# Performance work log

Measured on AMD Instinct MI355X. Metric: run time of the kernel, lower is better.

Reference implementation:

```python
import jax, jax.numpy as jnp
import numpy as np

WIDTH = 128


def setup_inputs() -> dict:
    key = jax.random.key(0)
    k_logits, k_w1, k_b1, k_w2, k_b2 = jax.random.split(key, 5)
    B, T, V = 32, 256, 4096
    logits = jax.random.normal(k_logits, (B, T, V), dtype=jnp.float32)
    # Linear(1, width): weight [width, 1] -> stored transposed as [1, width]
    w1 = jax.random.normal(k_w1, (1, WIDTH), dtype=jnp.float32) / jnp.sqrt(1.0)
    b1 = jax.random.normal(k_b1, (WIDTH,), dtype=jnp.float32) * 0.1
    # Linear(width, 1): weight [1, width] -> stored transposed as [width, 1]
    w2 = jax.random.normal(k_w2, (WIDTH, 1), dtype=jnp.float32) / jnp.sqrt(WIDTH)
    b2 = jax.random.normal(k_b2, (1,), dtype=jnp.float32) * 0.1
    return {"logits": logits, "w1": w1, "b1": b1, "w2": w2, "b2": b2}


def reference(logits, w1, b1, w2, b2):
    B, T, V = logits.shape
    logits_trim = logits[:, :-1, :]                       # [B, T-1, V]
    # entropy of softmax over the class dim; logits - logsumexp == log_softmax
    logp = jax.nn.log_softmax(logits_trim, axis=-1)       # [B, T-1, V]
    p = jnp.exp(logp)
    entropy = -jnp.sum(p * logp, axis=-1, keepdims=True)  # [B, T-1, 1]
    entropy_max = jnp.log(jnp.asarray(T, dtype=logits.dtype))  # log(num_steps)
    norm = 2.0 * entropy / entropy_max - 1.0              # [B, T-1, 1]
    # tiny 1 -> width -> 1 MLP
    hidden = jax.nn.relu(norm @ w1 + b1)                  # [B, T-1, width]
    lin = (2.0 * hidden) @ w2 + b2                        # [B, T-1, 1]
    # ns = [T-1, T-2, ..., 1]
    ns = jnp.arange(T - 1, 0, -1, dtype=logits.dtype).reshape(1, T - 1, 1)
    flags_trim = jax.nn.sigmoid(lin - jnp.log(ns))        # [B, T-1, 1]
    zeros = jnp.zeros((B, 1, 1), dtype=logits.dtype)
    ones = jnp.ones((B, 1, 1), dtype=logits.dtype)
    flags = jnp.concatenate([zeros, flags_trim, ones], axis=1)  # [B, T+1, 1]
    probabilities = jax.nn.softmax(logits, axis=2)        # [B, T, V]
    residuals = jnp.cumprod(1.0 - flags[:, :-1], axis=1)  # [B, T, 1] survival
    frequencies = probabilities * flags[:, 1:] * residuals  # [B, T, V]
    return frequencies
```

## Files before the change

### kernel.cpp

```cpp
#include <hip/hip_runtime.h>
#include <math.h>

#define T_DIM 256
#define V_DIM 4096
#define WIDTH 128

__device__ __forceinline__ float wave_max_f(float v) {
#pragma unroll
  for (int o = 32; o > 0; o >>= 1) v = fmaxf(v, __shfl_xor(v, o));
  return v;
}

__device__ __forceinline__ float wave_sum_f(float v) {
#pragma unroll
  for (int o = 32; o > 0; o >>= 1) v += __shfl_xor(v, o);
  return v;
}

__device__ __forceinline__ double wave_sum_d(double v) {
#pragma unroll
  for (int o = 32; o > 0; o >>= 1) v += __shfl_xor(v, o);
  return v;
}

__global__ __launch_bounds__(256) void row_stats(
    const float* __restrict__ logits,
    const float* __restrict__ w1, const float* __restrict__ b1,
    const float* __restrict__ w2, const float* __restrict__ b2,
    float* __restrict__ row_max, double* __restrict__ row_Z,
    double* __restrict__ row_flag) {
  const int row = blockIdx.x;
  const int t = row & (T_DIM - 1);
  const int tid = threadIdx.x;
  const int lane = tid & 63;
  const int wave = tid >> 6;

  const float4* src = (const float4*)(logits + (size_t)row * V_DIM);
  float4 xv[4];
#pragma unroll
  for (int k = 0; k < 4; ++k) xv[k] = src[tid + k * 256];

  float m = -INFINITY;
#pragma unroll
  for (int k = 0; k < 4; ++k)
    m = fmaxf(m, fmaxf(fmaxf(xv[k].x, xv[k].y), fmaxf(xv[k].z, xv[k].w)));
  m = wave_max_f(m);

  __shared__ float smax[4];
  __shared__ float szs[4], sss[4];
  if (lane == 0) smax[wave] = m;
  __syncthreads();
  m = fmaxf(fmaxf(smax[0], smax[1]), fmaxf(smax[2], smax[3]));

  float z = 0.f, s = 0.f;
#pragma unroll
  for (int k = 0; k < 4; ++k) {
    float vals[4] = {xv[k].x, xv[k].y, xv[k].z, xv[k].w};
#pragma unroll
    for (int j = 0; j < 4; ++j) {
      float sv = vals[j] - m;
      float ev = expf(sv);
      z += ev;
      s = fmaf(ev, sv, s);
    }
  }
  z = wave_sum_f(z);
  s = wave_sum_f(s);
  if (lane == 0) { szs[wave] = z; sss[wave] = s; }
  __syncthreads();

  if (wave == 0 && lane == 0) {
    double zd = (double)szs[0] + szs[1] + szs[2] + szs[3];
    double sd = (double)sss[0] + sss[1] + sss[2] + sss[3];
    row_max[row] = m;
    row_Z[row] = zd;
    if (t < T_DIM - 1) {
      double H = log(zd) - sd / zd;
      double nrm = 2.0 * H / log(256.0) - 1.0;
      double acc = 0.0;
#pragma unroll 4
      for (int j = 0; j < WIDTH; ++j) {
        double h = nrm * (double)w1[j] + (double)b1[j];
        h = h > 0.0 ? h : 0.0;
        acc += h * (double)w2[j];
      }
      double lin = 2.0 * acc + (double)b2[0];
      double xx = lin - log((double)(T_DIM - 1 - t));
      row_flag[row] = 1.0 / (1.0 + exp(-xx));
    }
  }
}

__global__ __launch_bounds__(64) void cumprod_scan(
    const double* __restrict__ row_Z, const double* __restrict__ row_flag,
    float* __restrict__ row_scale) {
  const int b = blockIdx.x;
  const int lane = threadIdx.x;
  __shared__ double fl[T_DIM];

  const double* fb = row_flag + (size_t)b * T_DIM;
  const double* Zb = row_Z + (size_t)b * T_DIM;

#pragma unroll
  for (int j = lane; j < T_DIM; j += 64) fl[j] = (j == T_DIM - 1) ? 1.0 : fb[j];
  __syncthreads();

  double loc[4];
  double p = 1.0;
#pragma unroll
  for (int j = 0; j < 4; ++j) {
    int t = lane * 4 + j;
    double flag_t = (t == 0) ? 0.0 : fl[t - 1];
    p *= (1.0 - flag_t);
    loc[j] = p;
  }
  double inc = p;
#pragma unroll
  for (int o = 1; o < 64; o <<= 1) {
    double up = __shfl_up(inc, o);
    if (lane >= o) inc *= up;
  }
  double exc = __shfl_up(inc, 1);
  if (lane == 0) exc = 1.0;

#pragma unroll
  for (int j = 0; j < 4; ++j) {
    int t = lane * 4 + j;
    double resid = exc * loc[j];
    row_scale[(size_t)b * T_DIM + t] = (float)(fl[t] * resid / Zb[t]);
  }
}

__global__ __launch_bounds__(256) void out_k(const float* __restrict__ logits,
                                             const float* __restrict__ row_max,
                                             const float* __restrict__ row_scale,
                                             float* __restrict__ out) {
  const int row = blockIdx.x;
  const int tid = threadIdx.x;
  const float m = row_max[row];
  const float sc = row_scale[row];
  const float4* src = (const float4*)(logits + (size_t)row * V_DIM);
  float4* dst = (float4*)(out + (size_t)row * V_DIM);
#pragma unroll
  for (int k = 0; k < 4; ++k) {
    float4 x = src[tid + k * 256];
    float4 o;
    o.x = expf(x.x - m) * sc;
    o.y = expf(x.y - m) * sc;
    o.z = expf(x.z - m) * sc;
    o.w = expf(x.w - m) * sc;
    dst[tid + k * 256] = o;
  }
}

extern "C" void kernel_launch(void* const* d_in, const int* in_sizes, int n_in,
                              void* d_out, int out_size, void* d_ws, size_t ws_size,
                              hipStream_t stream) {
  const float* logits = (const float*)d_in[0];
  const float* w1 = (const float*)d_in[1];
  const float* b1 = (const float*)d_in[2];
  const float* w2 = (const float*)d_in[3];
  const float* b2 = (const float*)d_in[4];
  float* out = (float*)d_out;

  const size_t nrows = (size_t)in_sizes[0] / V_DIM;
  const int Bn = (int)(nrows / T_DIM);

  double* row_Z = (double*)d_ws;
  double* row_flag = row_Z + nrows;
  float* row_max = (float*)(row_flag + nrows);
  float* row_scale = row_max + nrows;

  row_stats<<<(int)nrows, 256, 0, stream>>>(logits, w1, b1, w2, b2,
                                            row_max, row_Z, row_flag);
  cumprod_scan<<<Bn, 64, 0, stream>>>(row_Z, row_flag, row_scale);
  out_k<<<(int)nrows, 256, 0, stream>>>(logits, row_max, row_scale, out);
}
```

Before: 263.5 us.

## Fuse three kernels into one cooperative persistent kernel with grid syncs

Replaces the row-stats, cumprod-scan and output kernels with a single cooperative kernel of 512 blocks, each handling 16 rows, separated by two grid-wide syncs. The MLP flag computation is moved from one thread per row to 16 threads per block running in parallel, and output stores use nontemporal hints. The aim is to remove launch gaps and the serial tail of many tiny kernels. The cost is fewer resident blocks, so less latency hiding on the 134 MB streaming passes, plus the overhead of the grid barriers.

```diff
diff --git a/kernel.cpp b/kernel.cpp
--- a/kernel.cpp
+++ b/kernel.cpp
@@ -1,155 +1,160 @@
 #include <hip/hip_runtime.h>
+#include <hip/hip_cooperative_groups.h>
 #include <math.h>
+
+namespace cg = cooperative_groups;
 
 #define T_DIM 256
 #define V_DIM 4096
 #define WIDTH 128
+#define NBLK 512
+#define ROWS_PER_BLK 16
+
+typedef float floatx4 __attribute__((ext_vector_type(4)));
 
 __device__ __forceinline__ float wave_max_f(float v) {
 #pragma unroll
   for (int o = 32; o > 0; o >>= 1) v = fmaxf(v, __shfl_xor(v, o));
   return v;
 }
-
 __device__ __forceinline__ float wave_sum_f(float v) {
 #pragma unroll
   for (int o = 32; o > 0; o >>= 1) v += __shfl_xor(v, o);
   return v;
 }
 
-__device__ __forceinline__ double wave_sum_d(double v) {
-#pragma unroll
-  for (int o = 32; o > 0; o >>= 1) v += __shfl_xor(v, o);
-  return v;
-}
-
-__global__ __launch_bounds__(256) void row_stats(
+__global__ __launch_bounds__(256, 2) void fused(
     const float* __restrict__ logits,
     const float* __restrict__ w1, const float* __restrict__ b1,
     const float* __restrict__ w2, const float* __restrict__ b2,
+    float* __restrict__ out,
     float* __restrict__ row_max, double* __restrict__ row_Z,
-    double* __restrict__ row_flag) {
-  const int row = blockIdx.x;
-  const int t = row & (T_DIM - 1);
+    double* __restrict__ row_flag, float* __restrict__ row_scale) {
+  const int bid = blockIdx.x;
   const int tid = threadIdx.x;
   const int lane = tid & 63;
   const int wave = tid >> 6;
+  cg::grid_group grid = cg::this_grid();
 
-  const float4* src = (const float4*)(logits + (size_t)row * V_DIM);
-  float4 xv[4];
+  __shared__ float redM[4], redZ[4], redS[4];
+  __shared__ double sZ[ROWS_PER_BLK], sS[ROWS_PER_BLK];
+  __shared__ double fl[T_DIM];
+
+  for (int r = 0; r < ROWS_PER_BLK; ++r) {
+    const int row = bid * ROWS_PER_BLK + r;
+    const float4* src = (const float4*)(logits + (size_t)row * V_DIM);
+    float4 xv[4];
 #pragma unroll
-  for (int k = 0; k < 4; ++k) xv[k] = src[tid + k * 256];
+    for (int k = 0; k < 4; ++k) xv[k] = src[tid + k * 256];
 
-  float m = -INFINITY;
+    float m = -INFINITY;
 #pragma unroll
-  for (int k = 0; k < 4; ++k)
-    m = fmaxf(m, fmaxf(fmaxf(xv[k].x, xv[k].y), fmaxf(xv[k].z, xv[k].w)));
-  m = wave_max_f(m);
+    for (int k = 0; k < 4; ++k)
+      m = fmaxf(m, fmaxf(fmaxf(xv[k].x, xv[k].y), fmaxf(xv[k].z, xv[k].w)));
+    m = wave_max_f(m);
+    if (lane == 0) redM[wave] = m;
+    __syncthreads();
+    m = fmaxf(fmaxf(redM[0], redM[1]), fmaxf(redM[2], redM[3]));
 
-  __shared__ float smax[4];
-  __shared__ float szs[4], sss[4];
-  if (lane == 0) smax[wave] = m;
-  __syncthreads();
-  m = fmaxf(fmaxf(smax[0], smax[1]), fmaxf(smax[2], smax[3]));
+    float z = 0.f, s = 0.f;
+#pragma unroll
+    for (int k = 0; k < 4; ++k) {
+      float vals[4] = {xv[k].x, xv[k].y, xv[k].z, xv[k].w};
+#pragma unroll
+      for (int j = 0; j < 4; ++j) {
+        float sv = vals[j] - m;
+        float ev = expf(sv);
+        z += ev;
+        s = fmaf(ev, sv, s);
+      }
+    }
+    z = wave_sum_f(z);
+    s = wave_sum_f(s);
+    if (lane == 0) { redZ[wave] = z; redS[wave] = s; }
+    __syncthreads();
+    if (tid == 0) {
+      double zd = (double)redZ[0] + redZ[1] + redZ[2] + redZ[3];
+      double sd = (double)redS[0] + redS[1] + redS[2] + redS[3];
+      sZ[r] = zd; sS[r] = sd;
+      row_max[row] = m;
+      row_Z[row] = zd;
+    }
+    __syncthreads();
+  }
 
-  float z = 0.f, s = 0.f;
-#pragma unroll
-  for (int k = 0; k < 4; ++k) {
-    float vals[4] = {xv[k].x, xv[k].y, xv[k].z, xv[k].w};
-#pragma unroll
-    for (int j = 0; j < 4; ++j) {
-      float sv = vals[j] - m;
-      float ev = expf(sv);
-      z += ev;
-      s = fmaf(ev, sv, s);
-    }
-  }
-  z = wave_sum_f(z);
-  s = wave_sum_f(s);
-  if (lane == 0) { szs[wave] = z; sss[wave] = s; }
-  __syncthreads();
-
-  if (wave == 0 && lane == 0) {
-    double zd = (double)szs[0] + szs[1] + szs[2] + szs[3];
-    double sd = (double)sss[0] + sss[1] + sss[2] + sss[3];
-    row_max[row] = m;
-    row_Z[row] = zd;
+  if (tid < ROWS_PER_BLK) {
+    const int row = bid * ROWS_PER_BLK + tid;
+    const int t = row & (T_DIM - 1);
     if (t < T_DIM - 1) {
+      double zd = sZ[tid], sd = sS[tid];
       double H = log(zd) - sd / zd;
       double nrm = 2.0 * H / log(256.0) - 1.0;
       double acc = 0.0;
 #pragma unroll 4
       for (int j = 0; j < WIDTH; ++j) {
-        double h = nrm * (double)w1[j] + (double)b1[j];
+        double h = fma(nrm, (double)w1[j], (double)b1[j]);
         h = h > 0.0 ? h : 0.0;
-        acc += h * (double)w2[j];
+        acc = fma(h, (double)w2[j], acc);
       }
       double lin = 2.0 * acc + (double)b2[0];
       double xx = lin - log((double)(T_DIM - 1 - t));
       row_flag[row] = 1.0 / (1.0 + exp(-xx));
     }
   }
-}
 
-__global__ __launch_bounds__(64) void cumprod_scan(
-    const double* __restrict__ row_Z, const double* __restrict__ row_flag,
-    float* __restrict__ row_scale) {
-  const int b = blockIdx.x;
-  const int lane = threadIdx.x;
-  __shared__ double fl[T_DIM];
+  grid.sync();
 
-  const double* fb = row_flag + (size_t)b * T_DIM;
-  const double* Zb = row_Z + (size_t)b * T_DIM;
+  if (bid < 32 && wave == 0) {
+    const int b = bid;
+    const double* fb = row_flag + (size_t)b * T_DIM;
+    const double* Zb = row_Z + (size_t)b * T_DIM;
+#pragma unroll
+    for (int j = lane; j < T_DIM; j += 64)
+      fl[j] = (j == T_DIM - 1) ? 1.0 : fb[j];
 
+    double loc[4];
+    double p = 1.0;
 #pragma unroll
-  for (int j = lane; j < T_DIM; j += 64) fl[j] = (j == T_DIM - 1) ? 1.0 : fb[j];
-  __syncthreads();
+    for (int j = 0; j < 4; ++j) {
+      int t = lane * 4 + j;
+      double flag_t = (t == 0) ? 0.0 : fl[t - 1];
+      p *= (1.0 - flag_t);
+      loc[j] = p;
+    }
+    double inc = p;
+#pragma unroll
+    for (int o = 1; o < 64; o <<= 1) {
+      double up = __shfl_up(inc, o);
+      if (lane >= o) inc *= up;
+    }
+    double exc = __shfl_up(inc, 1);
+    if (lane == 0) exc = 1.0;
+#pragma unroll
+    for (int j = 0; j < 4; ++j) {
+      int t = lane * 4 + j;
+      double resid = exc * loc[j];
+      row_scale[(size_t)b * T_DIM + t] = (float)(fl[t] * resid / Zb[t]);
+    }
+  }
 
-  double loc[4];
-  double p = 1.0;
+  grid.sync();
+
+  for (int r = 0; r < ROWS_PER_BLK; ++r) {
+    const int row = bid * ROWS_PER_BLK + r;
+    const float m = row_max[row];
+    const float sc = row_scale[row];
+    const float4* src = (const float4*)(logits + (size_t)row * V_DIM);
+    floatx4* dst = (floatx4*)(out + (size_t)row * V_DIM);
 #pragma unroll
-  for (int j = 0; j < 4; ++j) {
-    int t = lane * 4 + j;
-    double flag_t = (t == 0) ? 0.0 : fl[t - 1];
-    p *= (1.0 - flag_t);
-    loc[j] = p;
-  }
-  double inc = p;
-#pragma unroll
-  for (int o = 1; o < 64; o <<= 1) {
-    double up = __shfl_up(inc, o);
-    if (lane >= o) inc *= up;
-  }
-  double exc = __shfl_up(inc, 1);
-  if (lane == 0) exc = 1.0;
-
-#pragma unroll
-  for (int j = 0; j < 4; ++j) {
-    int t = lane * 4 + j;
-    double resid = exc * loc[j];
-    row_scale[(size_t)b * T_DIM + t] = (float)(fl[t] * resid / Zb[t]);
-  }
-}
-
-__global__ __launch_bounds__(256) void out_k(const float* __restrict__ logits,
-                                             const float* __restrict__ row_max,
-                                             const float* __restrict__ row_scale,
-                                             float* __restrict__ out) {
-  const int row = blockIdx.x;
-  const int tid = threadIdx.x;
-  const float m = row_max[row];
-  const float sc = row_scale[row];
-  const float4* src = (const float4*)(logits + (size_t)row * V_DIM);
-  float4* dst = (float4*)(out + (size_t)row * V_DIM);
-#pragma unroll
-  for (int k = 0; k < 4; ++k) {
-    float4 x = src[tid + k * 256];
-    float4 o;
-    o.x = expf(x.x - m) * sc;
-    o.y = expf(x.y - m) * sc;
-    o.z = expf(x.z - m) * sc;
-    o.w = expf(x.w - m) * sc;
-    dst[tid + k * 256] = o;
+    for (int k = 0; k < 4; ++k) {
+      float4 x = src[tid + k * 256];
+      floatx4 o;
+      o.x = expf(x.x - m) * sc;
+      o.y = expf(x.y - m) * sc;
+      o.z = expf(x.z - m) * sc;
+      o.w = expf(x.w - m) * sc;
+      __builtin_nontemporal_store(o, &dst[tid + k * 256]);
+    }
   }
 }
 
@@ -164,15 +169,15 @@
   float* out = (float*)d_out;
 
   const size_t nrows = (size_t)in_sizes[0] / V_DIM;
-  const int Bn = (int)(nrows / T_DIM);
 
   double* row_Z = (double*)d_ws;
   double* row_flag = row_Z + nrows;
   float* row_max = (float*)(row_flag + nrows);
   float* row_scale = row_max + nrows;
 
-  row_stats<<<(int)nrows, 256, 0, stream>>>(logits, w1, b1, w2, b2,
-                                            row_max, row_Z, row_flag);
-  cumprod_scan<<<Bn, 64, 0, stream>>>(row_Z, row_flag, row_scale);
-  out_k<<<(int)nrows, 256, 0, stream>>>(logits, row_max, row_scale, out);
+  void* args[] = {(void*)&logits, (void*)&w1, (void*)&b1, (void*)&w2,
+                  (void*)&b2,     (void*)&out, (void*)&row_max,
+                  (void*)&row_Z,  (void*)&row_flag, (void*)&row_scale};
+  (void)hipLaunchCooperativeKernel((void*)fused, dim3(NBLK), dim3(256), args,
+                                   0, stream);
 }
```

Measured after the change: 367.8 us. +39.6%, slower.
